# Kernel optimization log

Hardware: AMD Instinct MI355X
Metric: run time of the kernel (lower is better)

The kernel has to match this reference:

```python
import jax, jax.numpy as jnp
import numpy as np

TSZ, BSZ, E, H = 1024, 8, 1024, 16


def setup_inputs() -> dict:
    key = jax.random.key(0)
    ks = jax.random.split(key, 7)
    s = 0.02
    return {
        "q": jax.random.normal(ks[0], (TSZ, BSZ, E), jnp.float32),
        "k": jax.random.normal(ks[1], (TSZ, BSZ, E), jnp.float32),
        "v": jax.random.normal(ks[2], (TSZ, BSZ, E), jnp.float32),
        "in_proj_weight": jax.random.normal(ks[3], (3 * E, E), jnp.float32) * s,
        "in_proj_bias": jax.random.normal(ks[4], (3 * E,), jnp.float32) * s,
        "out_proj_weight": jax.random.normal(ks[5], (E, E), jnp.float32) * s,
        "out_proj_bias": jax.random.normal(ks[6], (E,), jnp.float32) * s,
        "num_heads": H,
    }


def reference(q, k, v, in_proj_weight, in_proj_bias, out_proj_weight, out_proj_bias, num_heads):
    tsz, bsz, embed_dim = q.shape
    head_dim = embed_dim // num_heads
    scaling = float(head_dim) ** -0.5

    # in-projections (F.linear: x @ W.T + b), weight sliced into q/k/v chunks
    qp = q @ in_proj_weight[:embed_dim].T + in_proj_bias[:embed_dim]
    kp = k @ in_proj_weight[embed_dim:2 * embed_dim].T + in_proj_bias[embed_dim:2 * embed_dim]
    vp = v @ in_proj_weight[2 * embed_dim:].T + in_proj_bias[2 * embed_dim:]
    qp = qp * scaling

    # (tsz, bsz, E) -> (bsz*H, tsz, head_dim)
    def to_heads(x):
        return x.reshape(tsz, bsz * num_heads, head_dim).transpose(1, 0, 2)

    qh, kh, vh = to_heads(qp), to_heads(kp), to_heads(vp)

    # scaled dot-product attention (no mask, dropout p=0)
    scores = jnp.einsum('bqd,bkd->bqk', qh, kh)  # [bsz*H, tsz, tsz]
    weights = jax.nn.softmax(scores, axis=-1)
    attn = jnp.einsum('bqk,bkd->bqd', weights, vh)

    # back to (tsz, bsz, E), then out projection
    attn = attn.transpose(1, 0, 2).reshape(tsz, bsz, embed_dim)
    out = attn @ out_proj_weight.T + out_proj_bias
    return out
```

## Files before the change

kernel.cpp:

```cpp
#include <hip/hip_runtime.h>

typedef __bf16 bf16;
typedef __attribute__((ext_vector_type(8))) __bf16 v8bf;
typedef __attribute__((ext_vector_type(4))) __bf16 v4bf;
typedef __attribute__((ext_vector_type(4))) float f32x4;

static_assert(sizeof(v8bf) == 16, "v8bf must be 16B");

#define MFMA16(a, b, c) __builtin_amdgcn_mfma_f32_16x16x32_bf16((a), (b), (c), 0, 0, 0)

__device__ __forceinline__ void async_lds16(const bf16* g, bf16* l) {
  __builtin_amdgcn_global_load_lds(
      (__attribute__((address_space(1))) void*)(g),
      (__attribute__((address_space(3))) void*)(l), 16, 0, 0);
}

__global__ __launch_bounds__(256) void cvt_kernel(
    const float* __restrict__ q, const float* __restrict__ k,
    const float* __restrict__ v, const float* __restrict__ wi,
    const float* __restrict__ wo, bf16* __restrict__ xq, bf16* __restrict__ xk,
    bf16* __restrict__ xv, bf16* __restrict__ Wb, bf16* __restrict__ Wob) {
  int idx = blockIdx.x * 256 + threadIdx.x;
  const float4* src;
  v4bf* dst;
  int off;
  if (idx < 2097152)      { src = (const float4*)q;  dst = (v4bf*)xq;  off = idx; }
  else if (idx < 4194304) { src = (const float4*)k;  dst = (v4bf*)xk;  off = idx - 2097152; }
  else if (idx < 6291456) { src = (const float4*)v;  dst = (v4bf*)xv;  off = idx - 4194304; }
  else if (idx < 7077888) { src = (const float4*)wi; dst = (v4bf*)Wb;  off = idx - 6291456; }
  else                    { src = (const float4*)wo; dst = (v4bf*)Wob; off = idx - 7077888; }
  float4 f = src[off];
  v4bf b;
  b[0] = (bf16)f.x; b[1] = (bf16)f.y; b[2] = (bf16)f.z; b[3] = (bf16)f.w;
  dst[off] = b;
}

__global__ __launch_bounds__(256) void qkv_proj_kernel(
    const bf16* __restrict__ xq, const bf16* __restrict__ xk,
    const bf16* __restrict__ xv, const bf16* __restrict__ Wb,
    const float* __restrict__ bias, bf16* __restrict__ oq,
    bf16* __restrict__ ok, bf16* __restrict__ ov) {
  __shared__ bf16 Asm[128 * 32];
  __shared__ bf16 Bsm[128 * 32];
  const int L = blockIdx.x;
  const int rX = L & 7, rest = L >> 3;
  const int m0 = (rX * 8 + (rest & 7)) * 128;
  const int n0 = ((rest >> 3) & 7) * 128;
  const int c = rest >> 6;
  const bf16* X = (c == 0) ? xq : (c == 1) ? xk : xv;
  bf16* outp = (c == 0) ? oq : (c == 1) ? ok : ov;
  const int tid = threadIdx.x;
  const int w = tid >> 6, l = tid & 63, quad = l >> 4, lr = l & 15;
  const int wm = (w & 1) * 64, wn = (w >> 1) * 64;
  const int sw = quad ^ ((lr >> 1) & 3);
  const bf16* Wbase = Wb + ((size_t)(c * 1024 + n0)) * 1024;

  int srow[2], sk[2];
#pragma unroll
  for (int i = 0; i < 2; ++i) {
    const int chunk = w * 128 + i * 64 + l;
    srow[i] = chunk >> 2;
    sk[i] = ((chunk & 3) ^ ((srow[i] >> 1) & 3)) * 8;
  }

  f32x4 acc[4][4] = {};
  for (int kt = 0; kt < 32; ++kt) {
    const int k0 = kt * 32;
#pragma unroll
    for (int i = 0; i < 2; ++i) {
      async_lds16(X + (size_t)(m0 + srow[i]) * 1024 + k0 + sk[i],
                  &Asm[(w * 128 + i * 64) * 8]);
      async_lds16(Wbase + (size_t)srow[i] * 1024 + k0 + sk[i],
                  &Bsm[(w * 128 + i * 64) * 8]);
    }
    __syncthreads();
    v8bf af[4], bfm[4];
#pragma unroll
    for (int rt = 0; rt < 4; ++rt)
      af[rt] = *(const v8bf*)&Asm[(wm + rt * 16 + lr) * 32 + sw * 8];
#pragma unroll
    for (int ct = 0; ct < 4; ++ct)
      bfm[ct] = *(const v8bf*)&Bsm[(wn + ct * 16 + lr) * 32 + sw * 8];
#pragma unroll
    for (int rt = 0; rt < 4; ++rt)
#pragma unroll
      for (int ct = 0; ct < 4; ++ct)
        acc[rt][ct] = MFMA16(af[rt], bfm[ct], acc[rt][ct]);
    __syncthreads();
  }

  const float scale = (c == 0) ? 0.125f : 1.0f;
#pragma unroll
  for (int rt = 0; rt < 4; ++rt) {
#pragma unroll
    for (int ct = 0; ct < 4; ++ct) {
      const int n = n0 + wn + ct * 16 + lr;
      const float bn = bias[c * 1024 + n];
      const int h = n >> 6, d = n & 63;
#pragma unroll
      for (int j = 0; j < 4; ++j) {
        const int m = m0 + wm + rt * 16 + quad * 4 + j;
        const int t = m >> 3, b = m & 7;
        const float val = (acc[rt][ct][j] + bn) * scale;
        outp[((size_t)((b * 16 + h) * 1024 + t)) * 64 + d] = (bf16)val;
      }
    }
  }
}

__global__ __launch_bounds__(256) void transpose_v_kernel(const bf16* __restrict__ vin,
                                                          bf16* __restrict__ vout) {
  __shared__ bf16 tile[64][72];
  const int bh = blockIdx.x;
  const int t0 = blockIdx.y * 64;
  const int tid = threadIdx.x;
  const int row = tid >> 2, cg = (tid & 3) * 16;
  const bf16* src = vin + ((size_t)bh * 1024 + t0 + row) * 64 + cg;
#pragma unroll
  for (int i = 0; i < 2; ++i) {
    v8bf x = *(const v8bf*)(src + i * 8);
#pragma unroll
    for (int jj = 0; jj < 8; ++jj) tile[row][cg + i * 8 + jj] = x[jj];
  }
  __syncthreads();
  const int d = tid >> 2, tg = (tid & 3) * 16;
  bf16* dst = vout + ((size_t)bh * 64 + d) * 1024 + t0 + tg;
  v8bf o0, o1;
#pragma unroll
  for (int i = 0; i < 8; ++i) o0[i] = tile[tg + i][d];
#pragma unroll
  for (int i = 0; i < 8; ++i) o1[i] = tile[tg + 8 + i][d];
  *(v8bf*)dst = o0;
  *(v8bf*)(dst + 8) = o1;
}

#define KSTR 72
#define VSTR 136

__global__ __launch_bounds__(256, 3) void attn_kernel(const bf16* __restrict__ qh,
                                                      const bf16* __restrict__ kh,
                                                      const bf16* __restrict__ vT,
                                                      bf16* __restrict__ attn_out) {
  __shared__ bf16 Ksm[128 * KSTR];
  __shared__ bf16 Vsm[64 * VSTR];
  __shared__ bf16 Psm[4 * 16 * VSTR];
  const int L = blockIdx.x;
  const int bh = (L & 7) * 16 + ((L >> 3) & 15);
  const int t0 = (L >> 7) * 64;
  const int tid = threadIdx.x;
  const int w = tid >> 6, l = tid & 63, quad = l >> 4, lr = l & 15;
  const int qrow0 = t0 + w * 16;

  const bf16* khead = kh + (size_t)bh * 1024 * 64;
  const bf16* vhead = vT + (size_t)bh * 64 * 1024;

  const size_t qbase = ((size_t)bh * 1024 + qrow0 + lr) * 64 + quad * 8;
  const v8bf bq0 = *(const v8bf*)(qh + qbase);
  const v8bf bq1 = *(const v8bf*)(qh + qbase + 32);

  const int krow = tid >> 1, kd = (tid & 1) * 32;
  const int vrow = tid >> 2, vk = (tid & 3) * 32;
  const bf16* kg = khead + (size_t)krow * 64 + kd;
  const bf16* vg = vhead + (size_t)vrow * 1024 + vk;
  bf16* Kw = &Ksm[krow * KSTR + kd];
  bf16* Vw = &Vsm[vrow * VSTR + vk];
  bf16* Pw = &Psm[w * 16 * VSTR];

  v8bf kst[4], vst[4];
#pragma unroll
  for (int i = 0; i < 4; ++i) kst[i] = *(const v8bf*)(kg + i * 8);
#pragma unroll
  for (int i = 0; i < 4; ++i) vst[i] = *(const v8bf*)(vg + i * 8);

  float m_run = -3.0e38f, l_run = 0.0f;
  f32x4 oacc[4] = {};

  for (int c = 0; c < 8; ++c) {
    __syncthreads();
#pragma unroll
    for (int i = 0; i < 4; ++i) *(v8bf*)(Kw + i * 8) = kst[i];
#pragma unroll
    for (int i = 0; i < 4; ++i) *(v8bf*)(Vw + i * 8) = vst[i];
    __syncthreads();
    if (c < 7) {
      const bf16* kg2 = kg + (size_t)(c + 1) * 128 * 64;
      const bf16* vg2 = vg + (c + 1) * 128;
#pragma unroll
      for (int i = 0; i < 4; ++i) kst[i] = *(const v8bf*)(kg2 + i * 8);
#pragma unroll
      for (int i = 0; i < 4; ++i) vst[i] = *(const v8bf*)(vg2 + i * 8);
    }

    f32x4 s[8];
#pragma unroll
    for (int kt = 0; kt < 8; ++kt) {
      const v8bf ak0 = *(const v8bf*)&Ksm[(kt * 16 + lr) * KSTR + quad * 8];
      const v8bf ak1 = *(const v8bf*)&Ksm[(kt * 16 + lr) * KSTR + 32 + quad * 8];
      f32x4 a = {};
      a = MFMA16(ak0, bq0, a);
      a = MFMA16(ak1, bq1, a);
      s[kt] = a;
    }

    float mc = -3.0e38f;
#pragma unroll
    for (int kt = 0; kt < 8; ++kt)
#pragma unroll
      for (int j = 0; j < 4; ++j) mc = fmaxf(mc, s[kt][j]);
    mc = fmaxf(mc, __shfl_xor(mc, 16));
    mc = fmaxf(mc, __shfl_xor(mc, 32));
    const float m_new = fmaxf(m_run, mc);
    const float alpha = __expf(m_run - m_new);
    m_run = m_new;

    float sc = 0.0f;
#pragma unroll
    for (int kt = 0; kt < 8; ++kt) {
      v4bf pb;
#pragma unroll
      for (int j = 0; j < 4; ++j) {
        const float p = __expf(s[kt][j] - m_new);
        sc += p;
        pb[j] = (bf16)p;
      }
      *(v4bf*)(Pw + lr * VSTR + kt * 16 + quad * 4) = pb;
    }
    sc += __shfl_xor(sc, 16);
    sc += __shfl_xor(sc, 32);
    l_run = l_run * alpha + sc;

#pragma unroll
    for (int j = 0; j < 4; ++j) {
      const float aj = __shfl(alpha, quad * 4 + j);
#pragma unroll
      for (int dt = 0; dt < 4; ++dt) oacc[dt][j] *= aj;
    }

#pragma unroll
    for (int ks = 0; ks < 4; ++ks) {
      const v8bf pa = *(const v8bf*)(Pw + lr * VSTR + ks * 32 + quad * 8);
#pragma unroll
      for (int dt = 0; dt < 4; ++dt) {
        const v8bf vb = *(const v8bf*)&Vsm[(dt * 16 + lr) * VSTR + ks * 32 + quad * 8];
        oacc[dt] = MFMA16(pa, vb, oacc[dt]);
      }
    }
  }

  const float inv = 1.0f / l_run;
  const int b = bh >> 4, h = bh & 15;
#pragma unroll
  for (int j = 0; j < 4; ++j) {
    const float ij = __shfl(inv, quad * 4 + j);
    const int t = qrow0 + quad * 4 + j;
#pragma unroll
    for (int dt = 0; dt < 4; ++dt)
      attn_out[((size_t)(t * 8 + b)) * 1024 + h * 64 + dt * 16 + lr] =
          (bf16)(oacc[dt][j] * ij);
  }
}

__global__ __launch_bounds__(256) void out_proj_kernel(const bf16* __restrict__ A,
                                                       const bf16* __restrict__ Wob,
                                                       const float* __restrict__ bias,
                                                       float* __restrict__ out) {
  __shared__ bf16 Asm[128 * 32];
  __shared__ bf16 Bsm[128 * 32];
  const int L = blockIdx.x;
  const int m0 = ((L & 7) * 8 + ((L >> 3) & 7)) * 128;
  const int n0 = (L >> 6) * 128;
  const int tid = threadIdx.x;
  const int w = tid >> 6, l = tid & 63, quad = l >> 4, lr = l & 15;
  const int wm = (w & 1) * 64, wn = (w >> 1) * 64;
  const int sw = quad ^ ((lr >> 1) & 3);

  int srow[2], sk[2];
#pragma unroll
  for (int i = 0; i < 2; ++i) {
    const int chunk = w * 128 + i * 64 + l;
    srow[i] = chunk >> 2;
    sk[i] = ((chunk & 3) ^ ((srow[i] >> 1) & 3)) * 8;
  }

  f32x4 acc[4][4] = {};
  for (int kt = 0; kt < 32; ++kt) {
    const int k0 = kt * 32;
#pragma unroll
    for (int i = 0; i < 2; ++i) {
      async_lds16(A + (size_t)(m0 + srow[i]) * 1024 + k0 + sk[i],
                  &Asm[(w * 128 + i * 64) * 8]);
      async_lds16(Wob + (size_t)(n0 + srow[i]) * 1024 + k0 + sk[i],
                  &Bsm[(w * 128 + i * 64) * 8]);
    }
    __syncthreads();
    v8bf af[4], bfm[4];
#pragma unroll
    for (int rt = 0; rt < 4; ++rt)
      af[rt] = *(const v8bf*)&Asm[(wm + rt * 16 + lr) * 32 + sw * 8];
#pragma unroll
    for (int ct = 0; ct < 4; ++ct)
      bfm[ct] = *(const v8bf*)&Bsm[(wn + ct * 16 + lr) * 32 + sw * 8];
#pragma unroll
    for (int rt = 0; rt < 4; ++rt)
#pragma unroll
      for (int ct = 0; ct < 4; ++ct)
        acc[rt][ct] = MFMA16(af[rt], bfm[ct], acc[rt][ct]);
    __syncthreads();
  }

#pragma unroll
  for (int rt = 0; rt < 4; ++rt)
#pragma unroll
    for (int ct = 0; ct < 4; ++ct) {
      const int n = n0 + wn + ct * 16 + lr;
      const float bn = bias[n];
#pragma unroll
      for (int j = 0; j < 4; ++j) {
        const int m = m0 + wm + rt * 16 + quad * 4 + j;
        out[(size_t)m * 1024 + n] = acc[rt][ct][j] + bn;
      }
    }
}

extern "C" void kernel_launch(void* const* d_in, const int* in_sizes, int n_in,
                              void* d_out, int out_size, void* d_ws, size_t ws_size,
                              hipStream_t stream) {
  const float* q  = (const float*)d_in[0];
  const float* k  = (const float*)d_in[1];
  const float* v  = (const float*)d_in[2];
  const float* wi = (const float*)d_in[3];
  const float* bi = (const float*)d_in[4];
  const float* wo = (const float*)d_in[5];
  const float* bo = (const float*)d_in[6];
  float* out = (float*)d_out;
  char* ws = (char*)d_ws;
  const size_t MB = (size_t)1 << 20;
  bf16* Wb     = (bf16*)(ws + 0 * MB);
  bf16* Wob    = (bf16*)(ws + 6 * MB);
  bf16* wsq    = (bf16*)(ws + 8 * MB);
  bf16* wsk    = (bf16*)(ws + 24 * MB);
  bf16* wsv    = (bf16*)(ws + 40 * MB);
  bf16* xv     = (bf16*)(ws + 56 * MB);
  bf16* wsvT   = (bf16*)(ws + 56 * MB);
  bf16* xq     = (bf16*)d_out;
  bf16* xk     = (bf16*)((char*)d_out + 16 * MB);
  bf16* wsattn = wsv;

  cvt_kernel<<<dim3(28672), dim3(256), 0, stream>>>(q, k, v, wi, wo, xq, xk, xv, Wb, Wob);
  qkv_proj_kernel<<<dim3(1536), dim3(256), 0, stream>>>(xq, xk, xv, Wb, bi, wsq, wsk, wsv);
  transpose_v_kernel<<<dim3(128, 16), dim3(256), 0, stream>>>(wsv, wsvT);
  attn_kernel<<<dim3(2048), dim3(256), 0, stream>>>(wsq, wsk, wsvT, wsattn);
  out_proj_kernel<<<dim3(512), dim3(256), 0, stream>>>(wsattn, Wob, bo, out);
}
```

Before: 321.2 us.

## Process two query tiles per warp in attention to reuse K/V loads

Result: faster. 307.3 us (-4.3%).

```diff
diff --git a/kernel.cpp b/kernel.cpp
--- a/kernel.cpp
+++ b/kernel.cpp
@@ -137,26 +137,28 @@
 #define KSTR 72
 #define VSTR 136
 
-__global__ __launch_bounds__(256, 3) void attn_kernel(const bf16* __restrict__ qh,
+__global__ __launch_bounds__(256, 2) void attn_kernel(const bf16* __restrict__ qh,
                                                       const bf16* __restrict__ kh,
                                                       const bf16* __restrict__ vT,
                                                       bf16* __restrict__ attn_out) {
   __shared__ bf16 Ksm[128 * KSTR];
   __shared__ bf16 Vsm[64 * VSTR];
-  __shared__ bf16 Psm[4 * 16 * VSTR];
+  __shared__ bf16 Psm[128 * VSTR];
   const int L = blockIdx.x;
   const int bh = (L & 7) * 16 + ((L >> 3) & 15);
-  const int t0 = (L >> 7) * 64;
+  const int t0 = (L >> 7) * 128;
   const int tid = threadIdx.x;
   const int w = tid >> 6, l = tid & 63, quad = l >> 4, lr = l & 15;
-  const int qrow0 = t0 + w * 16;
+  const int qr0 = t0 + w * 32;
 
   const bf16* khead = kh + (size_t)bh * 1024 * 64;
   const bf16* vhead = vT + (size_t)bh * 64 * 1024;
 
-  const size_t qbase = ((size_t)bh * 1024 + qrow0 + lr) * 64 + quad * 8;
-  const v8bf bq0 = *(const v8bf*)(qh + qbase);
-  const v8bf bq1 = *(const v8bf*)(qh + qbase + 32);
+  const size_t qbase = ((size_t)bh * 1024 + qr0 + lr) * 64 + quad * 8;
+  const v8bf bq00 = *(const v8bf*)(qh + qbase);
+  const v8bf bq01 = *(const v8bf*)(qh + qbase + 32);
+  const v8bf bq10 = *(const v8bf*)(qh + qbase + 1024);
+  const v8bf bq11 = *(const v8bf*)(qh + qbase + 1024 + 32);
 
   const int krow = tid >> 1, kd = (tid & 1) * 32;
   const int vrow = tid >> 2, vk = (tid & 3) * 32;
@@ -164,7 +166,7 @@
   const bf16* vg = vhead + (size_t)vrow * 1024 + vk;
   bf16* Kw = &Ksm[krow * KSTR + kd];
   bf16* Vw = &Vsm[vrow * VSTR + vk];
-  bf16* Pw = &Psm[w * 16 * VSTR];
+  bf16* Pw = &Psm[w * 32 * VSTR];
 
   v8bf kst[4], vst[4];
 #pragma unroll
@@ -172,8 +174,9 @@
 #pragma unroll
   for (int i = 0; i < 4; ++i) vst[i] = *(const v8bf*)(vg + i * 8);
 
-  float m_run = -3.0e38f, l_run = 0.0f;
-  f32x4 oacc[4] = {};
+  float m_run0 = -3.0e38f, l_run0 = 0.0f;
+  float m_run1 = -3.0e38f, l_run1 = 0.0f;
+  f32x4 oacc0[4] = {}, oacc1[4] = {};
 
   for (int c = 0; c < 8; ++c) {
     __syncthreads();
@@ -191,72 +194,102 @@
       for (int i = 0; i < 4; ++i) vst[i] = *(const v8bf*)(vg2 + i * 8);
     }
 
-    f32x4 s[8];
+    f32x4 s0[8], s1[8];
 #pragma unroll
     for (int kt = 0; kt < 8; ++kt) {
       const v8bf ak0 = *(const v8bf*)&Ksm[(kt * 16 + lr) * KSTR + quad * 8];
       const v8bf ak1 = *(const v8bf*)&Ksm[(kt * 16 + lr) * KSTR + 32 + quad * 8];
       f32x4 a = {};
-      a = MFMA16(ak0, bq0, a);
-      a = MFMA16(ak1, bq1, a);
-      s[kt] = a;
-    }
-
-    float mc = -3.0e38f;
+      a = MFMA16(ak0, bq00, a);
+      a = MFMA16(ak1, bq01, a);
+      s0[kt] = a;
+      f32x4 b = {};
+      b = MFMA16(ak0, bq10, b);
+      b = MFMA16(ak1, bq11, b);
+      s1[kt] = b;
+    }
+
+    float mc0 = -3.0e38f, mc1 = -3.0e38f;
 #pragma unroll
     for (int kt = 0; kt < 8; ++kt)
 #pragma unroll
-      for (int j = 0; j < 4; ++j) mc = fmaxf(mc, s[kt][j]);
-    mc = fmaxf(mc, __shfl_xor(mc, 16));
-    mc = fmaxf(mc, __shfl_xor(mc, 32));
-    const float m_new = fmaxf(m_run, mc);
-    const float alpha = __expf(m_run - m_new);
-    m_run = m_new;
-
-    float sc = 0.0f;
+      for (int j = 0; j < 4; ++j) {
+        mc0 = fmaxf(mc0, s0[kt][j]);
+        mc1 = fmaxf(mc1, s1[kt][j]);
+      }
+    mc0 = fmaxf(mc0, __shfl_xor(mc0, 16));
+    mc0 = fmaxf(mc0, __shfl_xor(mc0, 32));
+    mc1 = fmaxf(mc1, __shfl_xor(mc1, 16));
+    mc1 = fmaxf(mc1, __shfl_xor(mc1, 32));
+    const float m_new0 = fmaxf(m_run0, mc0);
+    const float m_new1 = fmaxf(m_run1, mc1);
+    const float alpha0 = __expf(m_run0 - m_new0);
+    const float alpha1 = __expf(m_run1 - m_new1);
+    m_run0 = m_new0;
+    m_run1 = m_new1;
+
+    float sc0 = 0.0f, sc1 = 0.0f;
 #pragma unroll
     for (int kt = 0; kt < 8; ++kt) {
-      v4bf pb;
+      v4bf pb0, pb1;
 #pragma unroll
       for (int j = 0; j < 4; ++j) {
-        const float p = __expf(s[kt][j] - m_new);
-        sc += p;
-        pb[j] = (bf16)p;
-      }
-      *(v4bf*)(Pw + lr * VSTR + kt * 16 + quad * 4) = pb;
-    }
-    sc += __shfl_xor(sc, 16);
-    sc += __shfl_xor(sc, 32);
-    l_run = l_run * alpha + sc;
+        const float p0 = __expf(s0[kt][j] - m_new0);
+        const float p1 = __expf(s1[kt][j] - m_new1);
+        sc0 += p0;
+        sc1 += p1;
+        pb0[j] = (bf16)p0;
+        pb1[j] = (bf16)p1;
+      }
+      *(v4bf*)(Pw + lr * VSTR + kt * 16 + quad * 4) = pb0;
+      *(v4bf*)(Pw + (16 + lr) * VSTR + kt * 16 + quad * 4) = pb1;
+    }
+    sc0 += __shfl_xor(sc0, 16);
+    sc0 += __shfl_xor(sc0, 32);
+    sc1 += __shfl_xor(sc1, 16);
+    sc1 += __shfl_xor(sc1, 32);
+    l_run0 = l_run0 * alpha0 + sc0;
+    l_run1 = l_run1 * alpha1 + sc1;
 
 #pragma unroll
     for (int j = 0; j < 4; ++j) {
-      const float aj = __shfl(alpha, quad * 4 + j);
-#pragma unroll
-      for (int dt = 0; dt < 4; ++dt) oacc[dt][j] *= aj;
+      const float a0 = __shfl(alpha0, quad * 4 + j);
+      const float a1 = __shfl(alpha1, quad * 4 + j);
+#pragma unroll
+      for (int dt = 0; dt < 4; ++dt) {
+        oacc0[dt][j] *= a0;
+        oacc1[dt][j] *= a1;
+      }
     }
 
 #pragma unroll
     for (int ks = 0; ks < 4; ++ks) {
-      const v8bf pa = *(const v8bf*)(Pw + lr * VSTR + ks * 32 + quad * 8);
+      const v8bf pa0 = *(const v8bf*)(Pw + lr * VSTR + ks * 32 + quad * 8);
+      const v8bf pa1 = *(const v8bf*)(Pw + (16 + lr) * VSTR + ks * 32 + quad * 8);
 #pragma unroll
       for (int dt = 0; dt < 4; ++dt) {
         const v8bf vb = *(const v8bf*)&Vsm[(dt * 16 + lr) * VSTR + ks * 32 + quad * 8];
-        oacc[dt] = MFMA16(pa, vb, oacc[dt]);
-      }
-    }
-  }
-
-  const float inv = 1.0f / l_run;
+        oacc0[dt] = MFMA16(pa0, vb, oacc0[dt]);
+        oacc1[dt] = MFMA16(pa1, vb, oacc1[dt]);
+      }
+    }
+  }
+
+  const float inv0 = 1.0f / l_run0;
+  const float inv1 = 1.0f / l_run1;
   const int b = bh >> 4, h = bh & 15;
 #pragma unroll
   for (int j = 0; j < 4; ++j) {
-    const float ij = __shfl(inv, quad * 4 + j);
-    const int t = qrow0 + quad * 4 + j;
-#pragma unroll
-    for (int dt = 0; dt < 4; ++dt)
-      attn_out[((size_t)(t * 8 + b)) * 1024 + h * 64 + dt * 16 + lr] =
-          (bf16)(oacc[dt][j] * ij);
+    const float i0 = __shfl(inv0, quad * 4 + j);
+    const float i1 = __shfl(inv1, quad * 4 + j);
+    const int t0j = qr0 + quad * 4 + j;
+#pragma unroll
+    for (int dt = 0; dt < 4; ++dt) {
+      attn_out[((size_t)(t0j * 8 + b)) * 1024 + h * 64 + dt * 16 + lr] =
+          (bf16)(oacc0[dt][j] * i0);
+      attn_out[((size_t)((t0j + 16) * 8 + b)) * 1024 + h * 64 + dt * 16 + lr] =
+          (bf16)(oacc1[dt][j] * i1);
+    }
   }
 }
 
@@ -349,6 +382,6 @@
   cvt_kernel<<<dim3(28672), dim3(256), 0, stream>>>(q, k, v, wi, wo, xq, xk, xv, Wb, Wob);
   qkv_proj_kernel<<<dim3(1536), dim3(256), 0, stream>>>(xq, xk, xv, Wb, bi, wsq, wsk, wsv);
   transpose_v_kernel<<<dim3(128, 16), dim3(256), 0, stream>>>(wsv, wsvT);
-  attn_kernel<<<dim3(2048), dim3(256), 0, stream>>>(wsq, wsk, wsvT, wsattn);
+  attn_kernel<<<dim3(1024), dim3(256), 0, stream>>>(wsq, wsk, wsvT, wsattn);
   out_proj_kernel<<<dim3(512), dim3(256), 0, stream>>>(wsattn, Wob, bo, out);
 }
```
